# Optimization experiments

Hardware: AMD Instinct MI355X
Metric: run time of the kernel (lower is better)

## Reference

```python
import jax, jax.numpy as jnp
import numpy as np

N_FULL = 200000  # full-graph nodes
N_SUB = 80000    # subgraph nodes
E = 800000       # subgraph edges
IN = 128         # input feature dim
HD = 128         # hidden dim
LMAX = 5         # max ACT depth


def setup_inputs() -> dict:
    key = jax.random.key(0)
    ks = jax.random.split(key, 12)
    s = lambda i, shape: jax.random.normal(ks[i], shape, jnp.float32) * 0.05
    return dict(
        x_full=jax.random.normal(ks[0], (N_FULL, IN), jnp.float32),
        W_in=s(1, (HD, IN)), b_in=jnp.zeros((HD,), jnp.float32),
        W_l=s(2, (HD, HD)), b_l=jnp.zeros((HD,), jnp.float32),
        W_r=s(3, (HD, HD)),
        W_e1=s(4, (HD, 3 * HD)), b_e1=jnp.zeros((HD,), jnp.float32),
        W_e2=s(5, (1, HD)), b_e2=jnp.zeros((1,), jnp.float32),
        W_h1=s(6, (64, 2 * HD + 1)), b_h1=jnp.zeros((64,), jnp.float32),
        W_h2=s(7, (1, 64)), b_h2=jnp.zeros((1,), jnp.float32),
        subset=jax.random.randint(ks[8], (N_SUB,), 0, N_FULL),
        edge_index=jax.random.randint(ks[9], (2, E), 0, N_SUB),
    )


def reference(x_full, W_in, b_in, W_l, b_l, W_r, W_e1, b_e1, W_e2, b_e2,
              W_h1, b_h1, W_h2, b_h2, subset, edge_index):
    src, dst = edge_index[0], edge_index[1]
    # in-degree for mean aggregation (PyG SAGEConv default aggr='mean')
    deg = jax.ops.segment_sum(jnp.ones((E,), x_full.dtype), dst, num_segments=N_SUB)
    deg = jnp.maximum(deg, 1.0)[:, None]

    def sage_step(Hn):
        agg = jax.ops.segment_sum(Hn[src], dst, num_segments=N_SUB) / deg
        return jax.nn.relu(agg @ W_l.T + b_l + Hn @ W_r.T)

    # input projection of gathered subgraph features
    Hk = x_full[subset] @ W_in.T + b_in
    u_idx, v_idx = 0, 1  # mapping of (u, v) in relabeled subgraph

    alphas, scores = [], []
    p_not = jnp.float32(1.0)
    for depth_k in range(1, LMAX + 1):
        # incremental: one more shared SAGE step == k fresh steps from H0
        Hk = sage_step(Hk)
        h_u, h_v = Hk[u_idx], Hk[v_idx]
        feat = jnp.concatenate([h_u, h_v, h_u * h_v])            # [3*HD]
        score = jax.nn.relu(feat @ W_e1.T + b_e1) @ W_e2.T + b_e2  # [1]
        hin = jnp.concatenate([h_u, h_v, score])                  # [2*HD+1]
        p_halt = jax.nn.sigmoid(jax.nn.relu(hin @ W_h1.T + b_h1) @ W_h2.T + b_h2)[0]
        alphas.append(p_halt * p_not)
        scores.append(score[0])
        p_not = p_not * (1.0 - p_halt)

    alpha = jnp.stack(alphas)
    alpha = alpha / (alpha.sum() + 1e-8)
    scores_v = jnp.stack(scores)
    final_score = (alpha * scores_v).sum()
    depths = jnp.arange(1, LMAX + 1, dtype=jnp.float32)
    expected_depth = (alpha * depths).sum()
    return final_score, expected_depth, alpha
```

## Files before the change

### kernel.cpp

```cpp
#include <hip/hip_runtime.h>
#include <hip/hip_bf16.h>

#define N_FULL 200000
#define N_SUB  80000
#define E_NUM  800000
#define IN_DIM 128
#define HD     128
#define LMAX   5

#define NB_SCAN ((N_SUB + 255) / 256)


__global__ void init_all(int* __restrict__ cnt, int* __restrict__ cursor,
                         int* __restrict__ level) {
    int i = blockIdx.x * blockDim.x + threadIdx.x;
    if (i < N_SUB) {
        cnt[i] = 0;
        cursor[i] = 0;
        level[i] = (i < 2) ? 0 : 7;
    }
}

__global__ void count_deg(const int* __restrict__ dst, int* __restrict__ cnt) {
    int i = blockIdx.x * blockDim.x + threadIdx.x;
    if (i < E_NUM) atomicAdd(&cnt[dst[i]], 1);
}

__global__ void scan_block(const int* __restrict__ cnt, int* __restrict__ offs,
                           int* __restrict__ bsums) {
    __shared__ int s[256];
    int t = threadIdx.x;
    int i = blockIdx.x * 256 + t;
    int v = (i < N_SUB) ? cnt[i] : 0;
    s[t] = v;
    __syncthreads();
    for (int off = 1; off < 256; off <<= 1) {
        int x = (t >= off) ? s[t - off] : 0;
        __syncthreads();
        s[t] += x;
        __syncthreads();
    }
    if (i < N_SUB) offs[i] = s[t] - v;
    if (t == 255) bsums[blockIdx.x] = s[255];
}

__global__ void scan_sums(int* __restrict__ bsums) {
    __shared__ int s[512];
    int t = threadIdx.x;
    int v = (t < NB_SCAN) ? bsums[t] : 0;
    s[t] = v;
    __syncthreads();
    for (int off = 1; off < 512; off <<= 1) {
        int x = (t >= off) ? s[t - off] : 0;
        __syncthreads();
        s[t] += x;
        __syncthreads();
    }
    if (t < NB_SCAN) bsums[t] = s[t] - v;
}

__global__ void scan_add(int* __restrict__ offs, const int* __restrict__ bsums) {
    int i = blockIdx.x * 256 + threadIdx.x;
    if (i < N_SUB) offs[i] += bsums[blockIdx.x];
    if (i == 0) offs[N_SUB] = E_NUM;
}

__global__ void fill_csr(const int* __restrict__ src, const int* __restrict__ dst,
                         const int* __restrict__ offs, int* __restrict__ cursor,
                         int* __restrict__ csr) {
    int i = blockIdx.x * blockDim.x + threadIdx.x;
    if (i < E_NUM) {
        int d = dst[i];
        int p = atomicAdd(&cursor[d], 1);
        csr[offs[d] + p] = src[i];
    }
}


__global__ void bfs_pass(const int* __restrict__ src, const int* __restrict__ dst,
                         int* __restrict__ level, int t) {
    int i = blockIdx.x * blockDim.x + threadIdx.x;
    if (i >= E_NUM) return;
    int v = dst[i];
    if (level[v] == t) {
        int u = src[i];
        if (level[u] > t + 1) level[u] = t + 1;
    }
}


__global__ __launch_bounds__(256) void hist_levels(const int* __restrict__ level,
                                                   int* __restrict__ bhist) {
    __shared__ int h[8];
    int t = threadIdx.x;
    if (t < 8) h[t] = 0;
    __syncthreads();
    int i = blockIdx.x * 256 + t;
    if (i < N_SUB) {
        int l = level[i];
        if (l > 5) l = 6;
        atomicAdd(&h[l], 1);
    }
    __syncthreads();
    if (t < 8) bhist[blockIdx.x * 8 + t] = h[t];
}


__global__ void scan_hist(int* __restrict__ bhist, int* __restrict__ base,
                          int* __restrict__ cum) {
    __shared__ int tot[8];
    int t = threadIdx.x;
    if (t < 8) {
        int acc = 0;
        for (int b = 0; b < NB_SCAN; ++b) {
            int v = bhist[b * 8 + t];
            bhist[b * 8 + t] = acc;
            acc += v;
        }
        tot[t] = acc;
    }
    __syncthreads();
    if (t == 0) {
        int acc = 0;
        for (int l = 0; l <= 5; ++l) {
            base[l] = acc;
            acc += tot[l];
            cum[l] = acc;
        }
    }
}


__global__ __launch_bounds__(256) void emit_order(const int* __restrict__ level,
                                                  const int* __restrict__ bhist,
                                                  const int* __restrict__ base,
                                                  int* __restrict__ order) {
    __shared__ int woff[4][8];
    int t = threadIdx.x;
    int lane = t & 63, wv = t >> 6;
    int i = blockIdx.x * 256 + t;
    int l = 7;
    if (i < N_SUB) {
        l = level[i];
        if (l > 5) l = 6;
    }
    unsigned long long mybal = 0;
#pragma unroll
    for (int q = 0; q < 8; ++q) {
        unsigned long long b = __ballot(l == q);
        if (q == l) mybal = b;
        if (lane == 0) woff[wv][q] = (int)__popcll(b);
    }
    int inrank = (int)__popcll(mybal & ((1ull << lane) - 1ull));
    __syncthreads();
    if (t < 8) {
        int acc = 0;
        for (int w2 = 0; w2 < 4; ++w2) {
            int c = woff[w2][t];
            woff[w2][t] = acc;
            acc += c;
        }
    }
    __syncthreads();
    if (i < N_SUB && l <= 5) {
        int pos = base[l] + bhist[blockIdx.x * 8 + l] + woff[wv][l] + inrank;
        order[pos] = i;
    }
}


__global__ __launch_bounds__(256) void aggregate_list(
    const float* __restrict__ H, float* __restrict__ Out,
    const int* __restrict__ offs, const int* __restrict__ csr,
    const int* __restrict__ cnt, const int* __restrict__ order,
    const int* __restrict__ cumptr, int lvl) {
    int M = cumptr[lvl];
    int ngroups = (M + 3) >> 2;
    int wid = threadIdx.x >> 6, lane = threadIdx.x & 63;
    for (int g = blockIdx.x; g < ngroups; g += gridDim.x) {
        int ni = g * 4 + wid;
        if (ni >= M) continue;
        int node = order[ni];
        int beg = offs[node], end = offs[node + 1];
        float ax = 0.f, ay = 0.f;
        for (int j = beg; j < end; ++j) {
            int s = csr[j];
            float2 v = *(const float2*)(H + (size_t)s * HD + lane * 2);
            ax += v.x; ay += v.y;
        }
        int c = cnt[node];
        float inv = 1.0f / (float)(c > 1 ? c : 1);
        *(float2*)(Out + (size_t)node * HD + lane * 2) = make_float2(ax * inv, ay * inv);
    }
}


#define GBM 64
#define GBK 32

__global__ __launch_bounds__(256) void gemm_list(
    const float* __restrict__ A1, const float* __restrict__ A2,
    const float* __restrict__ W1, const float* __restrict__ W2,
    const float* __restrict__ bias, float* __restrict__ Out,
    const int* __restrict__ order, const int* __restrict__ gather,
    const int* __restrict__ cumptr, int lvl, int do_relu) {

    __shared__ __align__(16) float As[GBK][68];
    __shared__ __align__(16) float Ws[GBK][132];

    int M = cumptr[lvl];
    int ntiles = (M + GBM - 1) / GBM;
    int tid = threadIdx.x;
    int tx = tid & 15, ty = tid >> 4;
    int r0 = ty * 4;
    int c0 = tx * 4;
    int nchunk = A2 ? 8 : 4;

    for (int tile = blockIdx.x; tile < ntiles; tile += gridDim.x) {
        int row0 = tile * GBM;

        float acc[4][8];
#pragma unroll
        for (int i = 0; i < 4; ++i)
#pragma unroll
            for (int j = 0; j < 8; ++j) acc[i][j] = 0.f;

        for (int ch = 0; ch < nchunk; ++ch) {
            const float* Asrc = (ch < 4) ? A1 : A2;
            const float* Wsrc = (ch < 4) ? W1 : W2;
            int kbase = (ch & 3) * GBK;

#pragma unroll
            for (int it = 0; it < 2; ++it) {
                int idx = tid + it * 256;
                int m = idx >> 3, kq = idx & 7;
                int row = row0 + m;
                float4 v = make_float4(0.f, 0.f, 0.f, 0.f);
                if (row < M) {
                    int nr = order[row];
                    int ar = gather ? gather[nr] : nr;
                    v = *(const float4*)(Asrc + (size_t)ar * 128 + kbase + kq * 4);
                }
                As[kq * 4 + 0][m] = v.x;
                As[kq * 4 + 1][m] = v.y;
                As[kq * 4 + 2][m] = v.z;
                As[kq * 4 + 3][m] = v.w;
            }
#pragma unroll
            for (int it = 0; it < 4; ++it) {
                int idx = tid + it * 256;
                int n = idx >> 3, kq = idx & 7;
                float4 v = *(const float4*)(Wsrc + n * 128 + kbase + kq * 4);
                Ws[kq * 4 + 0][n] = v.x;
                Ws[kq * 4 + 1][n] = v.y;
                Ws[kq * 4 + 2][n] = v.z;
                Ws[kq * 4 + 3][n] = v.w;
            }
            __syncthreads();

#pragma unroll
            for (int kk = 0; kk < GBK; ++kk) {
                float4 a  = *(const float4*)&As[kk][r0];
                float4 w0 = *(const float4*)&Ws[kk][c0];
                float4 w1 = *(const float4*)&Ws[kk][c0 + 64];
                float av[4] = {a.x, a.y, a.z, a.w};
                float wv[8] = {w0.x, w0.y, w0.z, w0.w, w1.x, w1.y, w1.z, w1.w};
#pragma unroll
                for (int i = 0; i < 4; ++i)
#pragma unroll
                    for (int j = 0; j < 8; ++j)
                        acc[i][j] = fmaf(av[i], wv[j], acc[i][j]);
            }
            __syncthreads();
        }

#pragma unroll
        for (int i = 0; i < 4; ++i) {
            int row = row0 + r0 + i;
            if (row >= M) continue;
            int nr = order[row];
            float4 o0, o1;
            o0.x = acc[i][0] + bias[c0 + 0];
            o0.y = acc[i][1] + bias[c0 + 1];
            o0.z = acc[i][2] + bias[c0 + 2];
            o0.w = acc[i][3] + bias[c0 + 3];
            o1.x = acc[i][4] + bias[c0 + 64];
            o1.y = acc[i][5] + bias[c0 + 65];
            o1.z = acc[i][6] + bias[c0 + 66];
            o1.w = acc[i][7] + bias[c0 + 67];
            if (do_relu) {
                o0.x = fmaxf(o0.x, 0.f); o0.y = fmaxf(o0.y, 0.f);
                o0.z = fmaxf(o0.z, 0.f); o0.w = fmaxf(o0.w, 0.f);
                o1.x = fmaxf(o1.x, 0.f); o1.y = fmaxf(o1.y, 0.f);
                o1.z = fmaxf(o1.z, 0.f); o1.w = fmaxf(o1.w, 0.f);
            }
            *(float4*)(Out + (size_t)nr * 128 + c0) = o0;
            *(float4*)(Out + (size_t)nr * 128 + c0 + 64) = o1;
        }
    }
}


__global__ __launch_bounds__(256) void head_kernel(
    const float* __restrict__ H,
    const float* __restrict__ W_e1, const float* __restrict__ b_e1,
    const float* __restrict__ W_e2, const float* __restrict__ b_e2,
    const float* __restrict__ W_h1, const float* __restrict__ b_h1,
    const float* __restrict__ W_h2, const float* __restrict__ b_h2,
    float* __restrict__ head_out, int kidx) {

    __shared__ float feat[384];
    __shared__ float rowo[128];
    __shared__ float sc_sh;
    int t = threadIdx.x, lane = t & 63, wv = t >> 6;

    if (t < 128) {
        float a = H[t], b = H[128 + t];
        feat[t] = a;
        feat[128 + t] = b;
        feat[256 + t] = a * b;
    }
    __syncthreads();

    for (int r = wv; r < 128; r += 4) {
        const float* wr = W_e1 + r * 384;
        float acc = 0.f;
#pragma unroll
        for (int j = 0; j < 6; ++j)
            acc += feat[lane + 64 * j] * wr[lane + 64 * j];
        for (int off = 32; off; off >>= 1) acc += __shfl_down(acc, off);
        if (lane == 0) rowo[r] = fmaxf(acc + b_e1[r], 0.f) * W_e2[r];
    }
    __syncthreads();
    if (wv == 0) {
        float v = rowo[lane] + rowo[lane + 64];
        for (int off = 32; off; off >>= 1) v += __shfl_down(v, off);
        if (lane == 0) sc_sh = v + b_e2[0];
    }
    __syncthreads();
    float score = sc_sh;

    for (int r = wv; r < 64; r += 4) {
        const float* wh = W_h1 + r * 257;
        float acc = 0.f;
#pragma unroll
        for (int j = 0; j < 4; ++j)
            acc += feat[lane + 64 * j] * wh[lane + 64 * j];
        if (lane == 0) acc += score * wh[256];
        for (int off = 32; off; off >>= 1) acc += __shfl_down(acc, off);
        if (lane == 0) rowo[r] = fmaxf(acc + b_h1[r], 0.f) * W_h2[r];
    }
    __syncthreads();
    if (wv == 0) {
        float v = rowo[lane];
        for (int off = 32; off; off >>= 1) v += __shfl_down(v, off);
        if (lane == 0) {
            float p = 1.f / (1.f + expf(-(v + b_h2[0])));
            head_out[kidx * 2 + 0] = score;
            head_out[kidx * 2 + 1] = p;
        }
    }
}

__global__ void finalize(const float* __restrict__ head_out, float* __restrict__ out) {
    if (threadIdx.x == 0 && blockIdx.x == 0) {
        float a[LMAX];
        float p_not = 1.f, s = 0.f;
        for (int k = 0; k < LMAX; ++k) {
            float p = head_out[2 * k + 1];
            a[k] = p * p_not;
            p_not *= (1.f - p);
            s += a[k];
        }
        float inv = 1.f / (s + 1e-8f);
        float fs = 0.f, ed = 0.f;
        for (int k = 0; k < LMAX; ++k) {
            float al = a[k] * inv;
            out[2 + k] = al;
            fs += al * head_out[2 * k];
            ed += al * (float)(k + 1);
        }
        out[0] = fs;
        out[1] = ed;
    }
}


extern "C" void kernel_launch(void* const* d_in, const int* in_sizes, int n_in,
                              void* d_out, int out_size, void* d_ws, size_t ws_size,
                              hipStream_t stream) {
    const float* x_full = (const float*)d_in[0];
    const float* W_in  = (const float*)d_in[1];
    const float* b_in  = (const float*)d_in[2];
    const float* W_l   = (const float*)d_in[3];
    const float* b_l   = (const float*)d_in[4];
    const float* W_r   = (const float*)d_in[5];
    const float* W_e1  = (const float*)d_in[6];
    const float* b_e1  = (const float*)d_in[7];
    const float* W_e2  = (const float*)d_in[8];
    const float* b_e2  = (const float*)d_in[9];
    const float* W_h1  = (const float*)d_in[10];
    const float* b_h1  = (const float*)d_in[11];
    const float* W_h2  = (const float*)d_in[12];
    const float* b_h2  = (const float*)d_in[13];
    const int* subset  = (const int*)d_in[14];
    const int* edge    = (const int*)d_in[15];
    const int* esrc = edge;
    const int* edst = edge + E_NUM;

    char* w = (char*)d_ws;
    float* HA = (float*)w;      w += (size_t)N_SUB * HD * 4;
    float* HB = (float*)w;      w += (size_t)N_SUB * HD * 4;
    int* cnt = (int*)w;         w += (size_t)N_SUB * 4;
    int* offs = (int*)w;        w += (size_t)(N_SUB + 64) * 4;
    int* cursor = (int*)w;      w += (size_t)N_SUB * 4;
    int* csr = (int*)w;         w += (size_t)E_NUM * 4;
    int* level = (int*)w;       w += (size_t)N_SUB * 4;
    int* order = (int*)w;       w += (size_t)N_SUB * 4;
    int* bsums = (int*)w;       w += 4096;
    int* bhist = (int*)w;       w += (size_t)(NB_SCAN + 1) * 8 * 4;
    int* lvlbase = (int*)w;     w += 64;
    int* cum = (int*)w;         w += 64;
    float* head_out = (float*)w; w += 256;

    init_all<<<NB_SCAN, 256, 0, stream>>>(cnt, cursor, level);
    count_deg<<<(E_NUM + 255) / 256, 256, 0, stream>>>(edst, cnt);
    scan_block<<<NB_SCAN, 256, 0, stream>>>(cnt, offs, bsums);
    scan_sums<<<1, 512, 0, stream>>>(bsums);
    scan_add<<<NB_SCAN, 256, 0, stream>>>(offs, bsums);
    fill_csr<<<(E_NUM + 255) / 256, 256, 0, stream>>>(esrc, edst, offs, cursor, csr);

    for (int t = 0; t < 5; ++t)
        bfs_pass<<<(E_NUM + 255) / 256, 256, 0, stream>>>(esrc, edst, level, t);

    hist_levels<<<NB_SCAN, 256, 0, stream>>>(level, bhist);
    scan_hist<<<1, 64, 0, stream>>>(bhist, lvlbase, cum);
    emit_order<<<NB_SCAN, 256, 0, stream>>>(level, bhist, lvlbase, order);

    gemm_list<<<1250, 256, 0, stream>>>(
        x_full, nullptr, W_in, nullptr, b_in, HA, order, subset, cum, 5, 0);

    for (int k = 1; k <= LMAX; ++k) {
        int lvl = LMAX - k;
        int agrid  = (k == 1) ? 2048 : 96;
        int ggrid  = (k == 1) ? 640  : 96;
        aggregate_list<<<agrid, 256, 0, stream>>>(HA, HB, offs, csr, cnt, order, cum, lvl);
        gemm_list<<<ggrid, 256, 0, stream>>>(
            HB, HA, W_l, W_r, b_l, HA, order, nullptr, cum, lvl, 1);
        head_kernel<<<1, 256, 0, stream>>>(HA, W_e1, b_e1, W_e2, b_e2,
                                           W_h1, b_h1, W_h2, b_h2, head_out, k - 1);
    }
    finalize<<<1, 1, 0, stream>>>(head_out, (float*)d_out);
}
```

Measured before the change: 478.6 us.

## Fold input projection into first SAGE layer and use CSR-based BFS

Precomputes combined weights W_l·W_in and W_r·W_in plus a folded bias, so the first SAGE step aggregates raw gathered x_full rows through the subset map and skips the separate input-projection GEMM over level-5 nodes. BFS now walks CSR per frontier node over four passes instead of scanning all edges five times. The aggregation loop is unrolled by two to keep more gathers in flight. This adds a small weight-combination kernel and changes floating-point summation order.

```diff
diff --git a/kernel.cpp b/kernel.cpp
--- a/kernel.cpp
+++ b/kernel.cpp
@@ -77,13 +77,14 @@
 }
 
 
-__global__ void bfs_pass(const int* __restrict__ src, const int* __restrict__ dst,
-                         int* __restrict__ level, int t) {
+__global__ void bfs_csr(const int* __restrict__ offs, const int* __restrict__ csr,
+                        int* __restrict__ level, int t) {
     int i = blockIdx.x * blockDim.x + threadIdx.x;
-    if (i >= E_NUM) return;
-    int v = dst[i];
-    if (level[v] == t) {
-        int u = src[i];
+    if (i >= N_SUB) return;
+    if (level[i] != t) return;
+    int beg = offs[i], end = offs[i + 1];
+    for (int j = beg; j < end; ++j) {
+        int u = csr[j];
         if (level[u] > t + 1) level[u] = t + 1;
     }
 }
@@ -104,7 +105,6 @@
     __syncthreads();
     if (t < 8) bhist[blockIdx.x * 8 + t] = h[t];
 }
-
 
 __global__ void scan_hist(int* __restrict__ bhist, int* __restrict__ base,
                           int* __restrict__ cum) {
@@ -130,7 +130,6 @@
     }
 }
 
-
 __global__ __launch_bounds__(256) void emit_order(const int* __restrict__ level,
                                                   const int* __restrict__ bhist,
                                                   const int* __restrict__ base,
@@ -169,11 +168,37 @@
 }
 
 
+__global__ __launch_bounds__(256) void wcomb(
+    const float* __restrict__ W_l, const float* __restrict__ W_r,
+    const float* __restrict__ W_in, const float* __restrict__ b_in,
+    const float* __restrict__ b_l, float* __restrict__ Wc1,
+    float* __restrict__ Wc2, float* __restrict__ bc) {
+    int f = blockIdx.x;
+    int t = threadIdx.x;
+    int c = t & 127, p = t >> 7;
+    __shared__ float wl[128], wr[128];
+    if (t < 128) wl[t] = W_l[f * 128 + t];
+    else wr[t - 128] = W_r[f * 128 + (t - 128)];
+    __syncthreads();
+    const float* wrow = p ? wr : wl;
+    float acc = 0.f;
+#pragma unroll 8
+    for (int j = 0; j < 128; ++j)
+        acc = fmaf(wrow[j], W_in[j * 128 + c], acc);
+    (p ? Wc2 : Wc1)[f * 128 + c] = acc;
+    if (t < 64) {
+        float pa = (wl[t] + wr[t]) * b_in[t] + (wl[t + 64] + wr[t + 64]) * b_in[t + 64];
+        for (int off = 32; off; off >>= 1) pa += __shfl_down(pa, off);
+        if (t == 0) bc[f] = pa + b_l[f];
+    }
+}
+
+
 __global__ __launch_bounds__(256) void aggregate_list(
     const float* __restrict__ H, float* __restrict__ Out,
     const int* __restrict__ offs, const int* __restrict__ csr,
     const int* __restrict__ cnt, const int* __restrict__ order,
-    const int* __restrict__ cumptr, int lvl) {
+    const int* __restrict__ cumptr, int lvl, const int* __restrict__ srcmap) {
     int M = cumptr[lvl];
     int ngroups = (M + 3) >> 2;
     int wid = threadIdx.x >> 6, lane = threadIdx.x & 63;
@@ -182,15 +207,27 @@
         if (ni >= M) continue;
         int node = order[ni];
         int beg = offs[node], end = offs[node + 1];
-        float ax = 0.f, ay = 0.f;
-        for (int j = beg; j < end; ++j) {
-            int s = csr[j];
-            float2 v = *(const float2*)(H + (size_t)s * HD + lane * 2);
-            ax += v.x; ay += v.y;
+        float ax = 0.f, ay = 0.f, bx = 0.f, by = 0.f;
+        int j = beg;
+        for (; j + 1 < end; j += 2) {
+            int s0 = csr[j], s1 = csr[j + 1];
+            int r0 = srcmap ? srcmap[s0] : s0;
+            int r1 = srcmap ? srcmap[s1] : s1;
+            float2 v0 = *(const float2*)(H + (size_t)r0 * HD + lane * 2);
+            float2 v1 = *(const float2*)(H + (size_t)r1 * HD + lane * 2);
+            ax += v0.x; ay += v0.y;
+            bx += v1.x; by += v1.y;
+        }
+        if (j < end) {
+            int s0 = csr[j];
+            int r0 = srcmap ? srcmap[s0] : s0;
+            float2 v0 = *(const float2*)(H + (size_t)r0 * HD + lane * 2);
+            ax += v0.x; ay += v0.y;
         }
         int c = cnt[node];
         float inv = 1.0f / (float)(c > 1 ? c : 1);
-        *(float2*)(Out + (size_t)node * HD + lane * 2) = make_float2(ax * inv, ay * inv);
+        *(float2*)(Out + (size_t)node * HD + lane * 2) =
+            make_float2((ax + bx) * inv, (ay + by) * inv);
     }
 }
 
@@ -202,8 +239,9 @@
     const float* __restrict__ A1, const float* __restrict__ A2,
     const float* __restrict__ W1, const float* __restrict__ W2,
     const float* __restrict__ bias, float* __restrict__ Out,
-    const int* __restrict__ order, const int* __restrict__ gather,
-    const int* __restrict__ cumptr, int lvl, int do_relu) {
+    const int* __restrict__ order, const int* __restrict__ gatherA,
+    const int* __restrict__ gatherB, const int* __restrict__ cumptr,
+    int lvl, int do_relu) {
 
     __shared__ __align__(16) float As[GBK][68];
     __shared__ __align__(16) float Ws[GBK][132];
@@ -228,6 +266,7 @@
         for (int ch = 0; ch < nchunk; ++ch) {
             const float* Asrc = (ch < 4) ? A1 : A2;
             const float* Wsrc = (ch < 4) ? W1 : W2;
+            const int* gmap = (ch < 4) ? gatherA : gatherB;
             int kbase = (ch & 3) * GBK;
 
 #pragma unroll
@@ -238,7 +277,7 @@
                 float4 v = make_float4(0.f, 0.f, 0.f, 0.f);
                 if (row < M) {
                     int nr = order[row];
-                    int ar = gather ? gather[nr] : nr;
+                    int ar = gmap ? gmap[nr] : nr;
                     v = *(const float4*)(Asrc + (size_t)ar * 128 + kbase + kq * 4);
                 }
                 As[kq * 4 + 0][m] = v.x;
@@ -421,6 +460,9 @@
     int* bhist = (int*)w;       w += (size_t)(NB_SCAN + 1) * 8 * 4;
     int* lvlbase = (int*)w;     w += 64;
     int* cum = (int*)w;         w += 64;
+    float* Wc1 = (float*)w;     w += 128 * 128 * 4;
+    float* Wc2 = (float*)w;     w += 128 * 128 * 4;
+    float* bc = (float*)w;      w += 512;
     float* head_out = (float*)w; w += 256;
 
     init_all<<<NB_SCAN, 256, 0, stream>>>(cnt, cursor, level);
@@ -430,23 +472,26 @@
     scan_add<<<NB_SCAN, 256, 0, stream>>>(offs, bsums);
     fill_csr<<<(E_NUM + 255) / 256, 256, 0, stream>>>(esrc, edst, offs, cursor, csr);
 
-    for (int t = 0; t < 5; ++t)
-        bfs_pass<<<(E_NUM + 255) / 256, 256, 0, stream>>>(esrc, edst, level, t);
+    wcomb<<<128, 256, 0, stream>>>(W_l, W_r, W_in, b_in, b_l, Wc1, Wc2, bc);
+
+    for (int t = 0; t < 4; ++t)
+        bfs_csr<<<NB_SCAN, 256, 0, stream>>>(offs, csr, level, t);
 
     hist_levels<<<NB_SCAN, 256, 0, stream>>>(level, bhist);
     scan_hist<<<1, 64, 0, stream>>>(bhist, lvlbase, cum);
     emit_order<<<NB_SCAN, 256, 0, stream>>>(level, bhist, lvlbase, order);
 
-    gemm_list<<<1250, 256, 0, stream>>>(
-        x_full, nullptr, W_in, nullptr, b_in, HA, order, subset, cum, 5, 0);
-
-    for (int k = 1; k <= LMAX; ++k) {
+    aggregate_list<<<2048, 256, 0, stream>>>(x_full, HB, offs, csr, cnt, order, cum, 4, subset);
+    gemm_list<<<512, 256, 0, stream>>>(
+        HB, x_full, Wc1, Wc2, bc, HA, order, nullptr, subset, cum, 4, 1);
+    head_kernel<<<1, 256, 0, stream>>>(HA, W_e1, b_e1, W_e2, b_e2,
+                                       W_h1, b_h1, W_h2, b_h2, head_out, 0);
+
+    for (int k = 2; k <= LMAX; ++k) {
         int lvl = LMAX - k;
-        int agrid  = (k == 1) ? 2048 : 96;
-        int ggrid  = (k == 1) ? 640  : 96;
-        aggregate_list<<<agrid, 256, 0, stream>>>(HA, HB, offs, csr, cnt, order, cum, lvl);
-        gemm_list<<<ggrid, 256, 0, stream>>>(
-            HB, HA, W_l, W_r, b_l, HA, order, nullptr, cum, lvl, 1);
+        aggregate_list<<<96, 256, 0, stream>>>(HA, HB, offs, csr, cnt, order, cum, lvl, nullptr);
+        gemm_list<<<96, 256, 0, stream>>>(
+            HB, HA, W_l, W_r, b_l, HA, order, nullptr, nullptr, cum, lvl, 1);
         head_kernel<<<1, 256, 0, stream>>>(HA, W_e1, b_e1, W_e2, b_e2,
                                            W_h1, b_h1, W_h2, b_h2, head_out, k - 1);
     }
```

After: 449.7 us. 1.06x faster.
